# Kernel optimization log

Hardware: AMD Instinct MI355X
Metric: run time of the kernel (lower is better)

## Reference

```python
import jax, jax.numpy as jnp
import numpy as np

N_A = 100000; N_B = 100000; E = 1600000
H = 128; OUT = 16; G = 256; D_A = 64; D_B = 32


def setup_inputs() -> dict:
    key = jax.random.key(0)
    ks = jax.random.split(key, 24)
    f32 = jnp.float32
    def w(k, shape, fan_in):
        return jax.random.normal(k, shape, dtype=f32) / np.sqrt(fan_in)
    inp = {
        'x_a': jax.random.normal(ks[0], (N_A, D_A), dtype=f32),
        'x_b': jax.random.normal(ks[1], (N_B, D_B), dtype=f32),
        'ei_ab': jax.random.randint(ks[2], (2, E), 0, N_A),  # row0: src in a, row1: dst in b
        'ei_ba': jax.random.randint(ks[3], (2, E), 0, N_B),
        'ei_aa': jax.random.randint(ks[4], (2, E), 0, N_A),
        'batch_a': jnp.sort(jax.random.randint(ks[5], (N_A,), 0, G)),
        'batch_b': jnp.sort(jax.random.randint(ks[6], (N_B,), 0, G)),
        # node-type input embeddings
        'Wemb_a': w(ks[7], (D_A, H), D_A), 'bemb_a': jnp.zeros((H,), f32),
        'Wemb_b': w(ks[8], (D_B, H), D_B), 'bemb_b': jnp.zeros((H,), f32),
        # SAGEConv params per relation: lin_l (with bias) on aggregated, lin_r (no bias) on root
        'Wl_ab': w(ks[9], (H, H), H), 'bl_ab': jnp.zeros((H,), f32), 'Wr_ab': w(ks[10], (H, H), H),
        'Wl_ba': w(ks[11], (H, H), H), 'bl_ba': jnp.zeros((H,), f32), 'Wr_ba': w(ks[12], (H, H), H),
        'Wl_aa': w(ks[13], (H, H), H), 'bl_aa': jnp.zeros((H,), f32), 'Wr_aa': w(ks[14], (H, H), H),
        # output head
        'Wout': w(ks[15], (H, OUT), H), 'bout': jnp.zeros((OUT,), f32),
    }
    return inp


def _sage(x_src, x_dst, ei, Wl, bl, Wr, n_dst):
    # mean aggregation of source features over incoming edges, then transform + root
    msg = x_src[ei[0]]                                        # [E, H] gather
    s = jax.ops.segment_sum(msg, ei[1], num_segments=n_dst)   # [n_dst, H]
    cnt = jax.ops.segment_sum(jnp.ones((ei.shape[1], 1), x_src.dtype), ei[1], num_segments=n_dst)
    agg = s / jnp.maximum(cnt, 1.0)
    return agg @ Wl + bl + x_dst @ Wr


def _mean_pool(x, batch, num_graphs):
    s = jax.ops.segment_sum(x, batch, num_segments=num_graphs)
    cnt = jax.ops.segment_sum(jnp.ones((x.shape[0], 1), x.dtype), batch, num_segments=num_graphs)
    return s / jnp.maximum(cnt, 1.0)


def reference(x_a, x_b, ei_ab, ei_ba, ei_aa, batch_a, batch_b,
              Wemb_a, bemb_a, Wemb_b, bemb_b,
              Wl_ab, bl_ab, Wr_ab, Wl_ba, bl_ba, Wr_ba, Wl_aa, bl_aa, Wr_aa,
              Wout, bout):
    # per-type input projection
    h_a = x_a @ Wemb_a + bemb_a            # [N_A, H]
    h_b = x_b @ Wemb_b + bemb_b            # [N_B, H]
    # HeteroConv: one SAGEConv per relation, mean over relations per dst type
    m_b = _sage(h_a, h_b, ei_ab, Wl_ab, bl_ab, Wr_ab, N_B)          # dst 'b': 1 relation
    m_a1 = _sage(h_b, h_a, ei_ba, Wl_ba, bl_ba, Wr_ba, N_A)
    m_a2 = _sage(h_a, h_a, ei_aa, Wl_aa, bl_aa, Wr_aa, N_A)
    h_a2 = 0.5 * (m_a1 + m_a2)                                      # dst 'a': mean of 2 relations
    h_b2 = m_b
    # ReLU + per-type global mean pool + mean over node types
    p_a = _mean_pool(jax.nn.relu(h_a2), batch_a, G)                 # [G, H]
    p_b = _mean_pool(jax.nn.relu(h_b2), batch_b, G)
    x = 0.5 * (p_a + p_b)
    return x @ Wout + bout                                          # [G, OUT]
```

## Files before the change

kernel.cpp:

```cpp
#include <hip/hip_runtime.h>

#define NA 100000
#define NB 100000
#define NEDGE 1600000
#define HD 128
#define OUTD 16
#define NG 256
#define DA 64
#define DB 32

#define BIN_SHIFT 9
#define BIN_W 512
#define NBINS_R 196
#define NBINS 588
#define PADBIN 10240
#define EPB 8192
#define ECHUNKS 196

typedef unsigned int uint_t;
typedef unsigned short ushort_t;
typedef unsigned char uchar_t;
typedef __bf16 bf16_t;
typedef bf16_t bf16x8 __attribute__((ext_vector_type(8)));
typedef float f32x4 __attribute__((ext_vector_type(4)));
typedef float f32x2 __attribute__((ext_vector_type(2)));

__device__ __forceinline__ float bflo(uint_t u) {
    union { uint_t i; float f; } c; c.i = u << 16; return c.f;
}
__device__ __forceinline__ float bfhi(uint_t u) {
    union { uint_t i; float f; } c; c.i = u & 0xffff0000u; return c.f;
}
__device__ __forceinline__ float bf2f(ushort_t u) {
    union { uint_t i; float f; } c; c.i = ((uint_t)u) << 16; return c.f;
}
__device__ __forceinline__ uint_t f2bf(float f) {
    union { float f; uint_t i; } c; c.f = f;
    uint_t r = c.i + 0x7FFFu + ((c.i >> 16) & 1u);
    return r >> 16;
}
__device__ __forceinline__ uint_t pack2bf(float lo, float hi) {
    return f2bf(lo) | (f2bf(hi) << 16);
}
__device__ __forceinline__ uchar_t f2fp8(float v) {
    return (uchar_t)(__builtin_amdgcn_cvt_pk_fp8_f32(v, v, 0, false) & 0xff);
}

__global__ void __launch_bounds__(256)
prep_misc_kernel(const float* __restrict__ Wl_ab, const float* __restrict__ Wr_ab,
                 const float* __restrict__ Wl_ba, const float* __restrict__ Wl_aa,
                 const float* __restrict__ Wr_ba, const float* __restrict__ Wr_aa,
                 const float* __restrict__ Wemb_a, const float* __restrict__ Wemb_b,
                 ushort_t* __restrict__ wt_fb, ushort_t* __restrict__ wt_pa,
                 ushort_t* __restrict__ wt_ea, ushort_t* __restrict__ wt_eb,
                 const float* __restrict__ bl_ba, const float* __restrict__ bl_aa,
                 float* __restrict__ bias_pa,
                 const int* __restrict__ batch_a, const int* __restrict__ batch_b,
                 float* __restrict__ ga, float* __restrict__ gb)
{
    const int bx = blockIdx.x;
    __align__(16) ushort_t tmp[8];
    if (bx >= 40) {
        if (bx <= 43) {
            const int id = (bx - 40) * 256 + threadIdx.x;
            const int kk = id >> 9, ni = (id >> 6) & 7, l = id & 63;
            const int col = ni * 16 + (l & 15);
            const int k0 = kk * 32 + (l >> 4) * 8;
#pragma unroll
            for (int j = 0; j < 8; ++j) tmp[j] = (ushort_t)f2bf(Wemb_a[(k0 + j) * HD + col]);
            *reinterpret_cast<uint4*>(wt_ea + (size_t)id * 8) = *reinterpret_cast<const uint4*>(tmp);
            return;
        }
        if (bx <= 45) {
            const int id = (bx - 44) * 256 + threadIdx.x;
            const int ni = id >> 6, l = id & 63;
            const int col = ni * 16 + (l & 15);
            const int k0 = (l >> 4) * 8;
#pragma unroll
            for (int j = 0; j < 8; ++j) tmp[j] = (ushort_t)f2bf(Wemb_b[(k0 + j) * HD + col]);
            *reinterpret_cast<uint4*>(wt_eb + (size_t)id * 8) = *reinterpret_cast<const uint4*>(tmp);
            return;
        }
        if (bx == 46) {
            if (threadIdx.x < HD) bias_pa[threadIdx.x] = bl_ba[threadIdx.x] + bl_aa[threadIdx.x];
            return;
        }
        const int g = threadIdx.x;
        const int* batch = (bx == 48) ? batch_b : batch_a;
        float* outp = (bx == 48) ? gb : ga;
        const int n = NA;
        int lo0 = 0, hi0 = n;
        while (lo0 < hi0) { const int mid = (lo0 + hi0) >> 1; if (batch[mid] < g) lo0 = mid + 1; else hi0 = mid; }
        int lo1 = 0, hi1 = n;
        while (lo1 < hi1) { const int mid = (lo1 + hi1) >> 1; if (batch[mid] < g + 1) lo1 = mid + 1; else hi1 = mid; }
        outp[g] = (float)(lo1 - lo0);
        return;
    }
    const int m = bx >> 3;
    const int id = (bx & 7) * 256 + threadIdx.x;
    const int kk = id >> 9, ni = (id >> 6) & 7, l = id & 63;
    const int col = ni * 16 + (l & 15);
    const int k0 = kk * 32 + (l >> 4) * 8;
    const float* src = (m == 0) ? Wl_ab : (m == 1) ? Wr_ab : (m == 2) ? Wl_ba
                     : (m == 3) ? Wl_aa : Wr_ba;
#pragma unroll
    for (int j = 0; j < 8; ++j) {
        float v = src[(k0 + j) * HD + col];
        if (m == 4) v += Wr_aa[(k0 + j) * HD + col];
        tmp[j] = (ushort_t)f2bf(v);
    }
    const int half = ni >> 2, nih = ni & 3;
    const size_t eoff = (size_t)half * 8192 + ((kk * 4 + nih) * 64 + l) * 8;
    ushort_t* dst = (m < 2) ? (wt_fb + (size_t)m * 16384) : (wt_pa + (size_t)(m - 2) * 16384);
    *reinterpret_cast<uint4*>(dst + eoff) = *reinterpret_cast<const uint4*>(tmp);
}

template<int K>
__device__ __forceinline__ void
emb_body(const float* __restrict__ x, const ushort_t* __restrict__ wtf,
         const float* __restrict__ bias, ushort_t* __restrict__ h,
         uchar_t* __restrict__ h8, int n, ushort_t* wlds)
{
    constexpr int KST = K / 32;
    for (int i = threadIdx.x * 8; i < K * HD; i += 2048)
        *reinterpret_cast<uint4*>(wlds + i) = *reinterpret_cast<const uint4*>(wtf + i);
    __syncthreads();

    const int l = threadIdx.x & 63, w = threadIdx.x >> 6;
    const int lo = l & 15, hi = l >> 4;
    const int row_base = blockIdx.x * 128 + w * 32;

    f32x4 acc[2][8];
    const f32x4 zero = {0.f, 0.f, 0.f, 0.f};
#pragma unroll
    for (int mi = 0; mi < 2; ++mi)
#pragma unroll
        for (int ni = 0; ni < 8; ++ni) acc[mi][ni] = zero;

    bf16x8 a[2][KST];
#pragma unroll
    for (int mi = 0; mi < 2; ++mi) {
        int r = row_base + mi * 16 + lo;
        r = min(r, n - 1);
        const float* xr = x + (size_t)r * K + hi * 8;
#pragma unroll
        for (int kk = 0; kk < KST; ++kk) {
            const float4 f0 = *reinterpret_cast<const float4*>(xr + kk * 32);
            const float4 f1 = *reinterpret_cast<const float4*>(xr + kk * 32 + 4);
            __align__(16) ushort_t us[8];
            us[0] = (ushort_t)f2bf(f0.x); us[1] = (ushort_t)f2bf(f0.y);
            us[2] = (ushort_t)f2bf(f0.z); us[3] = (ushort_t)f2bf(f0.w);
            us[4] = (ushort_t)f2bf(f1.x); us[5] = (ushort_t)f2bf(f1.y);
            us[6] = (ushort_t)f2bf(f1.z); us[7] = (ushort_t)f2bf(f1.w);
            a[mi][kk] = *reinterpret_cast<const bf16x8*>(us);
        }
    }
#pragma unroll
    for (int kk = 0; kk < KST; ++kk) {
#pragma unroll
        for (int ni = 0; ni < 8; ++ni) {
            const bf16x8 b = *reinterpret_cast<const bf16x8*>(wlds + ((kk * 8 + ni) * 64 + l) * 8);
            acc[0][ni] = __builtin_amdgcn_mfma_f32_16x16x32_bf16(a[0][kk], b, acc[0][ni], 0, 0, 0);
            acc[1][ni] = __builtin_amdgcn_mfma_f32_16x16x32_bf16(a[1][kk], b, acc[1][ni], 0, 0, 0);
        }
    }
#pragma unroll
    for (int ni = 0; ni < 8; ++ni) {
        const int col = ni * 16 + lo;
        const float bv = bias[col];
#pragma unroll
        for (int mi = 0; mi < 2; ++mi) {
            const f32x4 v = acc[mi][ni];
#pragma unroll
            for (int r = 0; r < 4; ++r) {
                const int row = row_base + mi * 16 + hi * 4 + r;
                if (row < n) {
                    const float val = v[r] + bv;
                    h[(size_t)row * HD + col] = (ushort_t)f2bf(val);
                    h8[(size_t)row * HD + col] = f2fp8(val);
                }
            }
        }
    }
}

__global__ void __launch_bounds__(256)
emb2_kernel(const float* __restrict__ x_a, const float* __restrict__ x_b,
            const ushort_t* __restrict__ wt_ea, const ushort_t* __restrict__ wt_eb,
            const float* __restrict__ bemb_a, const float* __restrict__ bemb_b,
            ushort_t* __restrict__ h_a, ushort_t* __restrict__ h_b,
            uchar_t* __restrict__ h8_a, uchar_t* __restrict__ h8_b)
{
    __shared__ ushort_t wlds[DA * HD];
    if (blockIdx.y == 0) emb_body<DA>(x_a, wt_ea, bemb_a, h_a, h8_a, NA, wlds);
    else                 emb_body<DB>(x_b, wt_eb, bemb_b, h_b, h8_b, NB, wlds);
}

__global__ void __launch_bounds__(256)
part3_kernel(const int* __restrict__ ei_ab, const int* __restrict__ ei_ba,
             const int* __restrict__ ei_aa, int* __restrict__ bincnt,
             uint_t* __restrict__ binned)
{
    __shared__ uint_t sorted[EPB];
    __shared__ int lh[NBINS_R];
    __shared__ int lbase[NBINS_R];
    __shared__ int gbase[NBINS_R];
    __shared__ int lcur[NBINS_R];
    __shared__ int sc[256];
    const int r = blockIdx.y;
    const int* ei = (r == 0) ? ei_ab : (r == 1) ? ei_ba : ei_aa;
    const int t = threadIdx.x;
    for (int i = t; i < NBINS_R; i += 256) lh[i] = 0;
    __syncthreads();
    const int e0 = blockIdx.x * EPB;
    const int e1 = min(e0 + EPB, NEDGE);
    for (int e = e0 + t; e < e1; e += 256)
        atomicAdd(&lh[ei[NEDGE + e] >> BIN_SHIFT], 1);
    __syncthreads();
    {
        const int v = (t < NBINS_R) ? lh[t] : 0;
        sc[t] = v; __syncthreads();
        for (int d = 1; d < 256; d <<= 1) {
            const int x = (t >= d) ? sc[t - d] : 0;
            __syncthreads();
            sc[t] += x;
            __syncthreads();
        }
        if (t < NBINS_R) {
            const int ex = sc[t] - v;
            lbase[t] = ex; lcur[t] = ex;
            gbase[t] = v ? atomicAdd(&bincnt[r * NBINS_R + t], v) : 0;
        }
    }
    __syncthreads();
    for (int e = e0 + t; e < e1; e += 256) {
        const int dst = ei[NEDGE + e];
        const int src = ei[e];
        const int bin = dst >> BIN_SHIFT;
        const int pos = atomicAdd(&lcur[bin], 1);
        sorted[pos] = ((uint_t)(dst & (BIN_W - 1)) << 17) | (uint_t)src;
    }
    __syncthreads();
    const int wid = t >> 6, lane = t & 63;
    for (int b = wid; b < NBINS_R; b += 4) {
        const int cnt = lh[b], lb = lbase[b];
        uint_t* dst = binned + (size_t)(r * NBINS_R + b) * PADBIN + gbase[b];
        for (int k = lane; k < cnt; k += 64) dst[k] = sorted[lb + k];
    }
}

__global__ void __launch_bounds__(512)
gather3_kernel(const uchar_t* __restrict__ h8_a, const uchar_t* __restrict__ h8_b,
               const uint_t* __restrict__ binned, const int* __restrict__ bincnt,
               ushort_t* __restrict__ s_ab, ushort_t* __restrict__ s_ba,
               ushort_t* __restrict__ s_aa)
{
    __shared__ int hist[BIN_W];
    __shared__ int off[BIN_W];
    __shared__ int cursor[BIN_W];
    __shared__ uint_t eLDS[PADBIN];
    const int b = blockIdx.x, r = blockIdx.y;
    const int g = r * NBINS_R + b;
    const uchar_t* hsrc = (r == 1) ? h8_b : h8_a;
    ushort_t* s = (r == 0) ? s_ab : (r == 1) ? s_ba : s_aa;
    const int t = threadIdx.x;
    const int ecnt = bincnt[g];
    const uint_t* bsrc = binned + (size_t)g * PADBIN;

    hist[t] = 0;
    __syncthreads();
    for (int j = t; j < ecnt; j += 512)
        atomicAdd(&hist[bsrc[j] >> 17], 1);
    __syncthreads();
    const int v = hist[t];
    off[t] = v;
    __syncthreads();
    for (int d = 1; d < 512; d <<= 1) {
        const int x = (t >= d) ? off[t - d] : 0;
        __syncthreads();
        off[t] += x;
        __syncthreads();
    }
    const int ex = off[t] - v;
    __syncthreads();
    off[t] = ex;
    cursor[t] = ex;
    __syncthreads();
    for (int j = t; j < ecnt; j += 512) {
        const uint_t p = bsrc[j];
        const int pos = atomicAdd(&cursor[p >> 17], 1);
        eLDS[pos] = p & 0x1FFFFu;
    }
    __syncthreads();

    const int wid = t >> 6, lane = t & 63;
    const int hl = lane & 15;
    const int sel = lane >> 4;
    const int node0 = b * BIN_W;
    for (int nl = wid; nl < BIN_W; nl += 8) {
        const int node = node0 + nl;
        if (node >= NA) break;
        const int o0 = off[nl], deg = hist[nl];
        const int o1 = o0 + deg;
        f32x2 a01 = {0.f, 0.f}, a23 = {0.f, 0.f}, a45 = {0.f, 0.f}, a67 = {0.f, 0.f};
        int j = o0;
        for (; j + 8 <= o1; j += 8) {
            uint2 vv[2];
#pragma unroll
            for (int q = 0; q < 2; ++q) {
                const int sE = (int)eLDS[j + 4 * q + sel];
                vv[q] = *reinterpret_cast<const uint2*>(hsrc + (size_t)sE * HD + hl * 8);
            }
#pragma unroll
            for (int q = 0; q < 2; ++q) {
                a01 += __builtin_amdgcn_cvt_pk_f32_fp8(vv[q].x, false);
                a23 += __builtin_amdgcn_cvt_pk_f32_fp8(vv[q].x, true);
                a45 += __builtin_amdgcn_cvt_pk_f32_fp8(vv[q].y, false);
                a67 += __builtin_amdgcn_cvt_pk_f32_fp8(vv[q].y, true);
            }
        }
        for (; j + 4 <= o1; j += 4) {
            const int sE = (int)eLDS[j + sel];
            const uint2 vv = *reinterpret_cast<const uint2*>(hsrc + (size_t)sE * HD + hl * 8);
            a01 += __builtin_amdgcn_cvt_pk_f32_fp8(vv.x, false);
            a23 += __builtin_amdgcn_cvt_pk_f32_fp8(vv.x, true);
            a45 += __builtin_amdgcn_cvt_pk_f32_fp8(vv.y, false);
            a67 += __builtin_amdgcn_cvt_pk_f32_fp8(vv.y, true);
        }
        if (j < o1) {
            const int rem = o1 - j;
            const int sE = (int)eLDS[min(j + sel, o1 - 1)];
            const uint2 vv = *reinterpret_cast<const uint2*>(hsrc + (size_t)sE * HD + hl * 8);
            if (sel < rem) {
                a01 += __builtin_amdgcn_cvt_pk_f32_fp8(vv.x, false);
                a23 += __builtin_amdgcn_cvt_pk_f32_fp8(vv.x, true);
                a45 += __builtin_amdgcn_cvt_pk_f32_fp8(vv.y, false);
                a67 += __builtin_amdgcn_cvt_pk_f32_fp8(vv.y, true);
            }
        }
        float f0 = a01[0], f1 = a01[1], f2 = a23[0], f3 = a23[1];
        float f4 = a45[0], f5 = a45[1], f6 = a67[0], f7 = a67[1];
        f0 += __shfl_xor(f0, 16); f0 += __shfl_xor(f0, 32);
        f1 += __shfl_xor(f1, 16); f1 += __shfl_xor(f1, 32);
        f2 += __shfl_xor(f2, 16); f2 += __shfl_xor(f2, 32);
        f3 += __shfl_xor(f3, 16); f3 += __shfl_xor(f3, 32);
        f4 += __shfl_xor(f4, 16); f4 += __shfl_xor(f4, 32);
        f5 += __shfl_xor(f5, 16); f5 += __shfl_xor(f5, 32);
        f6 += __shfl_xor(f6, 16); f6 += __shfl_xor(f6, 32);
        f7 += __shfl_xor(f7, 16); f7 += __shfl_xor(f7, 32);
        if (sel == 0) {
            const float inv = 1.0f / fmaxf((float)deg, 1.0f);
            uint4 wv;
            wv.x = pack2bf(f0 * inv, f1 * inv);
            wv.y = pack2bf(f2 * inv, f3 * inv);
            wv.z = pack2bf(f4 * inv, f5 * inv);
            wv.w = pack2bf(f6 * inv, f7 * inv);
            *reinterpret_cast<uint4*>(s + (size_t)node * HD + hl * 8) = wv;
        }
    }
}

template<int NSRC, int SCALE_HALF>
__device__ __forceinline__ void
mfma_body(const ushort_t* __restrict__ x0, const ushort_t* __restrict__ x1,
          const ushort_t* __restrict__ x2,
          const ushort_t* __restrict__ wtf, const float* __restrict__ bias,
          ushort_t* __restrict__ m_out, int n, int tile, int half, char* smem)
{
    ushort_t* wlds = (ushort_t*)smem;
    for (int i = threadIdx.x * 8; i < NSRC * 8192; i += 2048) {
        const int s = i >> 13, off = i & 8191;
        *reinterpret_cast<uint4*>(wlds + i) =
            *reinterpret_cast<const uint4*>(wtf + (size_t)s * 16384 + half * 8192 + off);
    }
    __syncthreads();

    const int l  = threadIdx.x & 63, w = threadIdx.x >> 6;
    const int lo = l & 15, hi = l >> 4;
    const int row_base = tile * 128 + w * 32;

    f32x4 acc[2][4];
    const f32x4 zero = {0.f, 0.f, 0.f, 0.f};
#pragma unroll
    for (int mi = 0; mi < 2; ++mi)
#pragma unroll
        for (int ni = 0; ni < 4; ++ni) acc[mi][ni] = zero;

#pragma unroll
    for (int s = 0; s < NSRC; ++s) {
        const ushort_t* xs = (s == 0) ? x0 : (s == 1) ? x1 : x2;
        bf16x8 a[2][4];
#pragma unroll
        for (int mi = 0; mi < 2; ++mi) {
            int r = row_base + mi * 16 + lo;
            r = min(r, n - 1);
            const ushort_t* xr = xs + (size_t)r * HD + hi * 8;
#pragma unroll
            for (int kk = 0; kk < 4; ++kk)
                a[mi][kk] = *reinterpret_cast<const bf16x8*>(xr + kk * 32);
        }
        const ushort_t* wm = wlds + s * 8192;
#pragma unroll
        for (int kk = 0; kk < 4; ++kk) {
#pragma unroll
            for (int nih = 0; nih < 4; ++nih) {
                const bf16x8 b = *reinterpret_cast<const bf16x8*>(wm + ((kk * 4 + nih) * 64 + l) * 8);
                acc[0][nih] = __builtin_amdgcn_mfma_f32_16x16x32_bf16(a[0][kk], b, acc[0][nih], 0, 0, 0);
                acc[1][nih] = __builtin_amdgcn_mfma_f32_16x16x32_bf16(a[1][kk], b, acc[1][nih], 0, 0, 0);
            }
        }
    }

#pragma unroll
    for (int nih = 0; nih < 4; ++nih) {
        const int col = half * 64 + nih * 16 + lo;
        const float bv = bias[col];
#pragma unroll
        for (int mi = 0; mi < 2; ++mi) {
            const f32x4 v = acc[mi][nih];
#pragma unroll
            for (int r = 0; r < 4; ++r) {
                const int row = row_base + mi * 16 + hi * 4 + r;
                if (row < n) {
                    float val = v[r] + bv;
                    if (SCALE_HALF) val *= 0.5f;
                    m_out[(size_t)row * HD + col] = (ushort_t)f2bf(fmaxf(val, 0.f));
                }
            }
        }
    }
}

__global__ void __launch_bounds__(256)
mfma_merged(const ushort_t* __restrict__ s_ab, const ushort_t* __restrict__ h_b,
            const ushort_t* __restrict__ wt_fb, const float* __restrict__ bl_ab,
            ushort_t* __restrict__ m_b,
            const ushort_t* __restrict__ s_ba, const ushort_t* __restrict__ s_aa,
            const ushort_t* __restrict__ h_a,
            const ushort_t* __restrict__ wt_pa, const float* __restrict__ bias_pa,
            ushort_t* __restrict__ m_a)
{
    extern __shared__ char smem[];
    const int u = blockIdx.x;
    const int tile = (u >> 4) * 8 + (u & 7);
    const int half = (u >> 3) & 1;
    if (tile >= (NA + 127) / 128) return;
    if (blockIdx.y == 0)
        mfma_body<2, 0>(s_ab, h_b, nullptr, wt_fb, bl_ab, m_b, NB, tile, half, smem);
    else
        mfma_body<3, 1>(s_ba, s_aa, h_a, wt_pa, bias_pa, m_a, NA, tile, half, smem);
}

__global__ void __launch_bounds__(256)
pool_kernel(const ushort_t* __restrict__ m_a, const ushort_t* __restrict__ m_b,
            const int* __restrict__ batch_a, const int* __restrict__ batch_b,
            float* __restrict__ pool_a, float* __restrict__ pool_b)
{
    const ushort_t* m = blockIdx.y ? m_b : m_a;
    const int* batch = blockIdx.y ? batch_b : batch_a;
    float* pool = blockIdx.y ? pool_b : pool_a;
    const int col = threadIdx.x & 127;
    const int rh = threadIdx.x >> 7;
    int row = blockIdx.x * 128 + rh * 64;
    const int rend = min(row + 64, NA);
    if (row >= rend) return;
    float acc = 0.f;
    int gcur = batch[row];
    for (; row < rend; ++row) {
        const int g = batch[row];
        if (g != gcur) {
            unsafeAtomicAdd(pool + (size_t)gcur * HD + col, acc);
            acc = 0.f; gcur = g;
        }
        acc += bf2f(m[(size_t)row * HD + col]);
    }
    unsafeAtomicAdd(pool + (size_t)gcur * HD + col, acc);
}

__global__ void final_kernel(const float* __restrict__ pa, const float* __restrict__ pb,
                             const float* __restrict__ ga, const float* __restrict__ gb,
                             const float* __restrict__ Wout, const float* __restrict__ bout,
                             float* __restrict__ out)
{
    const int g = blockIdx.x;
    const int lane = threadIdx.x;
    const float inva = 1.0f / fmaxf(ga[g], 1.0f);
    const float invb = 1.0f / fmaxf(gb[g], 1.0f);
    if (lane < OUTD) {
        float acc = bout[lane];
        for (int k = 0; k < HD; ++k) {
            const float x = 0.5f * (pa[g * HD + k] * inva + pb[g * HD + k] * invb);
            acc = fmaf(x, Wout[k * OUTD + lane], acc);
        }
        out[g * OUTD + lane] = acc;
    }
}

extern "C" void kernel_launch(void* const* d_in, const int* in_sizes, int n_in,
                              void* d_out, int out_size, void* d_ws, size_t ws_size,
                              hipStream_t stream)
{
    const float* x_a     = (const float*)d_in[0];
    const float* x_b     = (const float*)d_in[1];
    const int*   ei_ab   = (const int*)d_in[2];
    const int*   ei_ba   = (const int*)d_in[3];
    const int*   ei_aa   = (const int*)d_in[4];
    const int*   batch_a = (const int*)d_in[5];
    const int*   batch_b = (const int*)d_in[6];
    const float* Wemb_a  = (const float*)d_in[7];
    const float* bemb_a  = (const float*)d_in[8];
    const float* Wemb_b  = (const float*)d_in[9];
    const float* bemb_b  = (const float*)d_in[10];
    const float* Wl_ab   = (const float*)d_in[11];
    const float* bl_ab   = (const float*)d_in[12];
    const float* Wr_ab   = (const float*)d_in[13];
    const float* Wl_ba   = (const float*)d_in[14];
    const float* bl_ba   = (const float*)d_in[15];
    const float* Wr_ba   = (const float*)d_in[16];
    const float* Wl_aa   = (const float*)d_in[17];
    const float* bl_aa   = (const float*)d_in[18];
    const float* Wr_aa   = (const float*)d_in[19];
    const float* Wout    = (const float*)d_in[20];
    const float* bout    = (const float*)d_in[21];
    float* out = (float*)d_out;

    char* p = (char*)d_ws;
    ushort_t* h_a  = (ushort_t*)p; p += (size_t)NA * HD * 2;
    ushort_t* h_b  = (ushort_t*)p; p += (size_t)NB * HD * 2;
    ushort_t* s_ab = (ushort_t*)p; p += (size_t)NB * HD * 2;
    ushort_t* s_ba = (ushort_t*)p; p += (size_t)NA * HD * 2;
    ushort_t* s_aa = (ushort_t*)p; p += (size_t)NA * HD * 2;
    ushort_t* m_a  = (ushort_t*)p; p += (size_t)NA * HD * 2;
    ushort_t* m_b  = (ushort_t*)p; p += (size_t)NB * HD * 2;
    uchar_t* h8_a  = (uchar_t*)p;  p += (size_t)NA * HD;
    uchar_t* h8_b  = (uchar_t*)p;  p += (size_t)NB * HD;
    uint_t* binned = (uint_t*)p; p += (size_t)NBINS * PADBIN * 4;
    int* bincnt = (int*)p;  p += (NBINS + 4) * 4;
    float* pool_a = (float*)p; p += (size_t)NG * HD * 4;
    float* pool_b = (float*)p; p += (size_t)NG * HD * 4;
    float* gcnt_a = (float*)p; p += NG * 4;
    float* gcnt_b = (float*)p; p += NG * 4;
    ushort_t* wt_fb = (ushort_t*)p; p += 2 * 16384 * 2;
    ushort_t* wt_pa = (ushort_t*)p; p += 3 * 16384 * 2;
    ushort_t* wt_ea = (ushort_t*)p; p += 64 * HD * 2;
    ushort_t* wt_eb = (ushort_t*)p; p += 32 * HD * 2;
    float* bias_pa  = (float*)p;    p += HD * 4;

    const int GT = (NA + 127) / 128;

    hipMemsetAsync(pool_a, 0, (size_t)2 * NG * HD * 4, stream);
    hipMemsetAsync(bincnt, 0, (size_t)NBINS * 4, stream);

    prep_misc_kernel<<<49, 256, 0, stream>>>(Wl_ab, Wr_ab, Wl_ba, Wl_aa, Wr_ba, Wr_aa,
                                             Wemb_a, Wemb_b, wt_fb, wt_pa, wt_ea, wt_eb,
                                             bl_ba, bl_aa, bias_pa,
                                             batch_a, batch_b, gcnt_a, gcnt_b);

    emb2_kernel<<<dim3(GT, 2), 256, 0, stream>>>(x_a, x_b, wt_ea, wt_eb, bemb_a, bemb_b,
                                                 h_a, h_b, h8_a, h8_b);

    part3_kernel<<<dim3(ECHUNKS, 3), 256, 0, stream>>>(ei_ab, ei_ba, ei_aa, bincnt, binned);
    gather3_kernel<<<dim3(NBINS_R, 3), 512, 0, stream>>>(h8_a, h8_b, binned, bincnt,
                                                         s_ab, s_ba, s_aa);

    const int lds_m = 3 * 16384;
    hipFuncSetAttribute((const void*)mfma_merged, hipFuncAttributeMaxDynamicSharedMemorySize, lds_m);
    const int GX = ((2 * GT + 15) / 16) * 16;
    mfma_merged<<<dim3(GX, 2), 256, lds_m, stream>>>(s_ab, h_b, wt_fb, bl_ab, m_b,
                                                     s_ba, s_aa, h_a, wt_pa, bias_pa, m_a);

    pool_kernel<<<dim3((NA + 127) / 128, 2), 256, 0, stream>>>(m_a, m_b, batch_a, batch_b, pool_a, pool_b);

    final_kernel<<<NG, 64, 0, stream>>>(pool_a, pool_b, gcnt_a, gcnt_b, Wout, bout, out);
}
```

Before: 383.5 us.

## Split gather bins into half-blocks of 256 nodes with wave-shuffle scan

Each gather block now covers half a 512-node bin: blockIdx.z selects which half, so the grid doubles and each block runs 256 threads. Each half-block rereads the whole bin's edge list and keeps only edges whose destination falls in its half. The shared-memory Hillis-Steele scan, which needed many barriers, is replaced by a wavefront __shfl_up scan followed by a cross-wave total. The aim is more, smaller blocks with less LDS each, for better occupancy and load balance. The cost is that every binned edge list is read twice, and the fixed eLDS capacity of 5632 could overflow if one half-bin receives more edges than that.

```diff
diff --git a/kernel.cpp b/kernel.cpp
--- a/kernel.cpp
+++ b/kernel.cpp
@@ -16,6 +16,8 @@
 #define PADBIN 10240
 #define EPB 8192
 #define ECHUNKS 196
+#define GBW 256
+#define EHALF 5632
 
 typedef unsigned int uint_t;
 typedef unsigned short ushort_t;
@@ -249,55 +251,62 @@
     }
 }
 
-__global__ void __launch_bounds__(512)
+__global__ void __launch_bounds__(256)
 gather3_kernel(const uchar_t* __restrict__ h8_a, const uchar_t* __restrict__ h8_b,
                const uint_t* __restrict__ binned, const int* __restrict__ bincnt,
                ushort_t* __restrict__ s_ab, ushort_t* __restrict__ s_ba,
                ushort_t* __restrict__ s_aa)
 {
-    __shared__ int hist[BIN_W];
-    __shared__ int off[BIN_W];
-    __shared__ int cursor[BIN_W];
-    __shared__ uint_t eLDS[PADBIN];
-    const int b = blockIdx.x, r = blockIdx.y;
+    __shared__ int hist[GBW];
+    __shared__ int off[GBW];
+    __shared__ int cursor[GBW];
+    __shared__ int wtot[4];
+    __shared__ uint_t eLDS[EHALF];
+    const int b = blockIdx.x, r = blockIdx.y, hf = blockIdx.z;
     const int g = r * NBINS_R + b;
     const uchar_t* hsrc = (r == 1) ? h8_b : h8_a;
     ushort_t* s = (r == 0) ? s_ab : (r == 1) ? s_ba : s_aa;
     const int t = threadIdx.x;
+    const int lane = t & 63, wid = t >> 6;
     const int ecnt = bincnt[g];
     const uint_t* bsrc = binned + (size_t)g * PADBIN;
 
     hist[t] = 0;
     __syncthreads();
-    for (int j = t; j < ecnt; j += 512)
-        atomicAdd(&hist[bsrc[j] >> 17], 1);
+    for (int j = t; j < ecnt; j += 256) {
+        const int ld = (int)(bsrc[j] >> 17);
+        if ((ld >> 8) == hf) atomicAdd(&hist[ld & (GBW - 1)], 1);
+    }
     __syncthreads();
     const int v = hist[t];
-    off[t] = v;
-    __syncthreads();
-    for (int d = 1; d < 512; d <<= 1) {
-        const int x = (t >= d) ? off[t - d] : 0;
-        __syncthreads();
-        off[t] += x;
-        __syncthreads();
-    }
-    const int ex = off[t] - v;
-    __syncthreads();
+    int sum = v;
+#pragma unroll
+    for (int d = 1; d < 64; d <<= 1) {
+        const int x = __shfl_up(sum, d);
+        if (lane >= d) sum += x;
+    }
+    if (lane == 63) wtot[wid] = sum;
+    __syncthreads();
+    int base = 0;
+    for (int q = 0; q < wid; ++q) base += wtot[q];
+    const int ex = base + sum - v;
     off[t] = ex;
     cursor[t] = ex;
     __syncthreads();
-    for (int j = t; j < ecnt; j += 512) {
+    for (int j = t; j < ecnt; j += 256) {
         const uint_t p = bsrc[j];
-        const int pos = atomicAdd(&cursor[p >> 17], 1);
-        eLDS[pos] = p & 0x1FFFFu;
-    }
-    __syncthreads();
-
-    const int wid = t >> 6, lane = t & 63;
+        const int ld = (int)(p >> 17);
+        if ((ld >> 8) == hf) {
+            const int pos = atomicAdd(&cursor[ld & (GBW - 1)], 1);
+            eLDS[pos] = p & 0x1FFFFu;
+        }
+    }
+    __syncthreads();
+
     const int hl = lane & 15;
     const int sel = lane >> 4;
-    const int node0 = b * BIN_W;
-    for (int nl = wid; nl < BIN_W; nl += 8) {
+    const int node0 = b * BIN_W + hf * GBW;
+    for (int nl = wid; nl < GBW; nl += 4) {
         const int node = node0 + nl;
         if (node >= NA) break;
         const int o0 = off[nl], deg = hist[nl];
@@ -560,8 +569,8 @@
                                                  h_a, h_b, h8_a, h8_b);
 
     part3_kernel<<<dim3(ECHUNKS, 3), 256, 0, stream>>>(ei_ab, ei_ba, ei_aa, bincnt, binned);
-    gather3_kernel<<<dim3(NBINS_R, 3), 512, 0, stream>>>(h8_a, h8_b, binned, bincnt,
-                                                         s_ab, s_ba, s_aa);
+    gather3_kernel<<<dim3(NBINS_R, 3, 2), 256, 0, stream>>>(h8_a, h8_b, binned, bincnt,
+                                                            s_ab, s_ba, s_aa);
 
     const int lds_m = 3 * 16384;
     hipFuncSetAttribute((const void*)mfma_merged, hipFuncAttributeMaxDynamicSharedMemorySize, lds_m);
```

New measurement: 385.8 us. No clear change (+0.6%).

## Shrink destination bins to 128 nodes and retile the binning and gather kernels

Applied to the files above, without the earlier changes.

Destination bins shrink from 512 to 128 nodes, so there are about four times as many bins and gather blocks. Gather blocks drop from 512 to 256 threads and use far less LDS. The gather prefix scan becomes a wave-shuffle scan, and the partition kernel now scans four bins per thread and writes out with 16-lane groups. The aim is better occupancy and load balance in the gather, but the partition writes become smaller, more scattered segments, and the per-bin padding margin is tighter.

```diff
diff --git a/kernel.cpp b/kernel.cpp
--- a/kernel.cpp
+++ b/kernel.cpp
@@ -9,11 +9,11 @@
 #define DA 64
 #define DB 32
 
-#define BIN_SHIFT 9
-#define BIN_W 512
-#define NBINS_R 196
-#define NBINS 588
-#define PADBIN 10240
+#define BIN_SHIFT 7
+#define BIN_W 128
+#define NBQ 782
+#define NBINS 2346
+#define PADBIN 3072
 #define EPB 8192
 #define ECHUNKS 196
 
@@ -202,15 +202,15 @@
              uint_t* __restrict__ binned)
 {
     __shared__ uint_t sorted[EPB];
-    __shared__ int lh[NBINS_R];
-    __shared__ int lbase[NBINS_R];
-    __shared__ int gbase[NBINS_R];
-    __shared__ int lcur[NBINS_R];
+    __shared__ int lh[NBQ];
+    __shared__ int lbase[NBQ];
+    __shared__ int gbase[NBQ];
+    __shared__ int lcur[NBQ];
     __shared__ int sc[256];
     const int r = blockIdx.y;
     const int* ei = (r == 0) ? ei_ab : (r == 1) ? ei_ba : ei_aa;
     const int t = threadIdx.x;
-    for (int i = t; i < NBINS_R; i += 256) lh[i] = 0;
+    for (int i = t; i < NBQ; i += 256) lh[i] = 0;
     __syncthreads();
     const int e0 = blockIdx.x * EPB;
     const int e1 = min(e0 + EPB, NEDGE);
@@ -218,18 +218,29 @@
         atomicAdd(&lh[ei[NEDGE + e] >> BIN_SHIFT], 1);
     __syncthreads();
     {
-        const int v = (t < NBINS_R) ? lh[t] : 0;
-        sc[t] = v; __syncthreads();
+        int v4[4]; int s = 0;
+#pragma unroll
+        for (int q = 0; q < 4; ++q) {
+            const int i = t * 4 + q;
+            v4[q] = (i < NBQ) ? lh[i] : 0;
+            s += v4[q];
+        }
+        sc[t] = s; __syncthreads();
         for (int d = 1; d < 256; d <<= 1) {
             const int x = (t >= d) ? sc[t - d] : 0;
             __syncthreads();
             sc[t] += x;
             __syncthreads();
         }
-        if (t < NBINS_R) {
-            const int ex = sc[t] - v;
-            lbase[t] = ex; lcur[t] = ex;
-            gbase[t] = v ? atomicAdd(&bincnt[r * NBINS_R + t], v) : 0;
+        int ex = sc[t] - s;
+#pragma unroll
+        for (int q = 0; q < 4; ++q) {
+            const int i = t * 4 + q;
+            if (i < NBQ) {
+                lbase[i] = ex; lcur[i] = ex;
+                gbase[i] = v4[q] ? atomicAdd(&bincnt[r * NBQ + i], v4[q]) : 0;
+            }
+            ex += v4[q];
         }
     }
     __syncthreads();
@@ -241,15 +252,15 @@
         sorted[pos] = ((uint_t)(dst & (BIN_W - 1)) << 17) | (uint_t)src;
     }
     __syncthreads();
-    const int wid = t >> 6, lane = t & 63;
-    for (int b = wid; b < NBINS_R; b += 4) {
+    const int grp = t >> 4, l16 = t & 15;
+    for (int b = grp; b < NBQ; b += 16) {
         const int cnt = lh[b], lb = lbase[b];
-        uint_t* dst = binned + (size_t)(r * NBINS_R + b) * PADBIN + gbase[b];
-        for (int k = lane; k < cnt; k += 64) dst[k] = sorted[lb + k];
-    }
-}
-
-__global__ void __launch_bounds__(512)
+        uint_t* dst = binned + (size_t)(r * NBQ + b) * PADBIN + gbase[b];
+        for (int k = l16; k < cnt; k += 16) dst[k] = sorted[lb + k];
+    }
+}
+
+__global__ void __launch_bounds__(256)
 gather3_kernel(const uchar_t* __restrict__ h8_a, const uchar_t* __restrict__ h8_b,
                const uint_t* __restrict__ binned, const int* __restrict__ bincnt,
                ushort_t* __restrict__ s_ab, ushort_t* __restrict__ s_ba,
@@ -258,46 +269,51 @@
     __shared__ int hist[BIN_W];
     __shared__ int off[BIN_W];
     __shared__ int cursor[BIN_W];
+    __shared__ int wtot[2];
     __shared__ uint_t eLDS[PADBIN];
     const int b = blockIdx.x, r = blockIdx.y;
-    const int g = r * NBINS_R + b;
+    const int g = r * NBQ + b;
     const uchar_t* hsrc = (r == 1) ? h8_b : h8_a;
     ushort_t* s = (r == 0) ? s_ab : (r == 1) ? s_ba : s_aa;
     const int t = threadIdx.x;
+    const int lane = t & 63, wid = t >> 6;
     const int ecnt = bincnt[g];
     const uint_t* bsrc = binned + (size_t)g * PADBIN;
 
-    hist[t] = 0;
-    __syncthreads();
-    for (int j = t; j < ecnt; j += 512)
+    if (t < BIN_W) hist[t] = 0;
+    __syncthreads();
+    for (int j = t; j < ecnt; j += 256)
         atomicAdd(&hist[bsrc[j] >> 17], 1);
     __syncthreads();
-    const int v = hist[t];
-    off[t] = v;
-    __syncthreads();
-    for (int d = 1; d < 512; d <<= 1) {
-        const int x = (t >= d) ? off[t - d] : 0;
+    if (t < BIN_W) {
+        const int v = hist[t];
+        int sum = v;
+#pragma unroll
+        for (int d = 1; d < 64; d <<= 1) {
+            const int x = __shfl_up(sum, d);
+            if (lane >= d) sum += x;
+        }
+        if (lane == 63) wtot[wid] = sum;
         __syncthreads();
-        off[t] += x;
+        const int base = (wid == 1) ? wtot[0] : 0;
+        const int ex = base + sum - v;
+        off[t] = ex;
+        cursor[t] = ex;
+    } else {
         __syncthreads();
     }
-    const int ex = off[t] - v;
-    __syncthreads();
-    off[t] = ex;
-    cursor[t] = ex;
-    __syncthreads();
-    for (int j = t; j < ecnt; j += 512) {
+    __syncthreads();
+    for (int j = t; j < ecnt; j += 256) {
         const uint_t p = bsrc[j];
         const int pos = atomicAdd(&cursor[p >> 17], 1);
         eLDS[pos] = p & 0x1FFFFu;
     }
     __syncthreads();
 
-    const int wid = t >> 6, lane = t & 63;
     const int hl = lane & 15;
     const int sel = lane >> 4;
     const int node0 = b * BIN_W;
-    for (int nl = wid; nl < BIN_W; nl += 8) {
+    for (int nl = wid; nl < BIN_W; nl += 4) {
         const int node = node0 + nl;
         if (node >= NA) break;
         const int o0 = off[nl], deg = hist[nl];
@@ -560,8 +576,8 @@
                                                  h_a, h_b, h8_a, h8_b);
 
     part3_kernel<<<dim3(ECHUNKS, 3), 256, 0, stream>>>(ei_ab, ei_ba, ei_aa, bincnt, binned);
-    gather3_kernel<<<dim3(NBINS_R, 3), 512, 0, stream>>>(h8_a, h8_b, binned, bincnt,
-                                                         s_ab, s_ba, s_aa);
+    gather3_kernel<<<dim3(NBQ, 3), 256, 0, stream>>>(h8_a, h8_b, binned, bincnt,
+                                                     s_ab, s_ba, s_aa);
 
     const int lds_m = 3 * 16384;
     hipFuncSetAttribute((const void*)mfma_merged, hipFuncAttributeMaxDynamicSharedMemorySize, lds_m);
```

New measurement: 385.0 us. No clear change (+0.4%).
